# Optimization experiments

Measured on AMD Instinct MI355X. Metric: run time of the kernel, lower is better.

Reference implementation:

```python
import jax, jax.numpy as jnp
import numpy as np

H = 128  # hidden size
D = 257  # input size


def _lstm(x, h0, c0, Wih, Whh, bih, bhh):
    """Single-layer batch-first LSTM, PyTorch gate order (i, f, g, o).
    x: [N, T, D_in]; h0, c0: [N, H]. Returns (ys [N,T,H], hT, cT)."""
    # Precompute the input contribution for all timesteps at once.
    pre = jnp.einsum('ntd,gd->ntg', x, Wih) + bih + bhh  # [N, T, 4H]

    def step(carry, g_t):
        h, c = carry
        gates = g_t + h @ Whh.T  # [N, 4H]
        i, f, g, o = jnp.split(gates, 4, axis=-1)
        c = jax.nn.sigmoid(f) * c + jax.nn.sigmoid(i) * jnp.tanh(g)
        h = jax.nn.sigmoid(o) * jnp.tanh(c)
        return (h, c), h

    (hT, cT), ys = jax.lax.scan(step, (h0, c0), jnp.swapaxes(pre, 0, 1))
    return jnp.swapaxes(ys, 0, 1), hT, cT


def setup_inputs() -> dict:
    key = jax.random.key(0)
    ks = jax.random.split(key, 12)
    N, T = 64, 1000
    s1 = 1.0 / np.sqrt(H)
    inp = {
        'x': jax.random.normal(ks[0], (N, T, D), jnp.float32),
        'in_states': jax.random.normal(ks[1], (1, 4 * N, H), jnp.float32),
        'Wih1': jax.random.uniform(ks[2], (4 * H, D), jnp.float32, -s1, s1),
        'Whh1': jax.random.uniform(ks[3], (4 * H, H), jnp.float32, -s1, s1),
        'bih1': jax.random.uniform(ks[4], (4 * H,), jnp.float32, -s1, s1),
        'bhh1': jax.random.uniform(ks[5], (4 * H,), jnp.float32, -s1, s1),
        'Wih2': jax.random.uniform(ks[6], (4 * H, H), jnp.float32, -s1, s1),
        'Whh2': jax.random.uniform(ks[7], (4 * H, H), jnp.float32, -s1, s1),
        'bih2': jax.random.uniform(ks[8], (4 * H,), jnp.float32, -s1, s1),
        'bhh2': jax.random.uniform(ks[9], (4 * H,), jnp.float32, -s1, s1),
        'Wd': jax.random.uniform(ks[10], (D, H), jnp.float32, -s1, s1),
        'bd': jax.random.uniform(ks[11], (D,), jnp.float32, -s1, s1),
    }
    return inp


def reference(x, in_states, Wih1, Whh1, bih1, bhh1, Wih2, Whh2, bih2, bhh2, Wd, bd):
    # in_states: [1, 4N, H] -> four [1, N, H] chunks: h1, c1, h2, c2
    h1_in, c1_in, h2_in, c2_in = jnp.split(in_states, 4, axis=1)
    x1, h1, c1 = _lstm(x, h1_in[0], c1_in[0], Wih1, Whh1, bih1, bhh1)
    # dropout is identity in eval/streaming inference
    x2, h2, c2 = _lstm(x1, h2_in[0], c2_in[0], Wih2, Whh2, bih2, bhh2)
    mask = jax.nn.sigmoid(jnp.einsum('nth,dh->ntd', x2, Wd) + bd)
    out_states = jnp.concatenate([h1[None], c1[None], h2[None], c2[None]], axis=1)
    return mask, out_states
```

## Files before the change

### kernel.cpp

```cpp
#include <hip/hip_runtime.h>
#include <hip/hip_bf16.h>
#include <math.h>

#define NBATCH 64
#define TSEQ   1000
#define DIN    257
#define HID    128
#define GATES  512
#define CH     8
#define NCHUNK 125

typedef _Float16 h2    __attribute__((ext_vector_type(2)));
typedef _Float16 h4    __attribute__((ext_vector_type(4)));
typedef _Float16 half8 __attribute__((ext_vector_type(8)));
typedef float    f32x4 __attribute__((ext_vector_type(4)));

__device__ __forceinline__ float fast_sigmoid(float x) {
    return __builtin_amdgcn_rcpf(1.f + __expf(-x));
}
__device__ __forceinline__ float fast_tanh(float x) {
    const float e = __expf(2.f * x);
    return 1.f - 2.f * __builtin_amdgcn_rcpf(e + 1.f);
}
__device__ __forceinline__ void wait_flag(const int* f, int need) {
    while (__hip_atomic_load(f, __ATOMIC_ACQUIRE, __HIP_MEMORY_SCOPE_AGENT) < need)
        __builtin_amdgcn_s_sleep(2);
}

#define BM 128
#define BN 64
#define BK 64
#define LDK 88

template<int ACT>
__global__ __launch_bounds__(256) void gemm_mfma(
    const float* __restrict__ A, const float* __restrict__ W,
    const float* __restrict__ b1, const float* __restrict__ b2,
    float* __restrict__ C, int M, int K, int Ncols)
{
    __shared__ _Float16 As[BM][LDK];
    __shared__ _Float16 Ws[BN][LDK];

    const int tid  = threadIdx.x;
    const int wave = tid >> 6;
    const int lane = tid & 63;
    const int r    = lane & 15;
    const int q    = lane >> 4;
    const int m0   = blockIdx.y * BM;
    const int n0   = blockIdx.x * BN;
    const int wm   = (wave >> 1) * 64;
    const int wn   = (wave & 1) * 32;

    const int r16 = tid >> 4;
    const int c4  = (tid & 15) * 4;

    f32x4 acc[4][2];
#pragma unroll
    for (int i = 0; i < 4; ++i)
#pragma unroll
        for (int j = 0; j < 2; ++j) acc[i][j] = f32x4{0.f, 0.f, 0.f, 0.f};

    for (int kc = 0; kc < K; kc += BK) {
        const int kg = kc + c4;
        const bool vec_ok = (kg + 4 <= K);

#pragma unroll
        for (int it = 0; it < 8; ++it) {
            const int row = it * 16 + r16;
            const float* src = A + (size_t)(m0 + row) * K + kg;
            _Float16 tmp[4];
            if (vec_ok) {
                const float4 u = *(const float4*)src;
                tmp[0] = (_Float16)u.x; tmp[1] = (_Float16)u.y;
                tmp[2] = (_Float16)u.z; tmp[3] = (_Float16)u.w;
            } else {
#pragma unroll
                for (int j = 0; j < 4; ++j)
                    tmp[j] = (kg + j < K) ? (_Float16)src[j] : (_Float16)0.f;
            }
            *(h4*)&As[row][c4] = *(h4*)tmp;
        }
#pragma unroll
        for (int it = 0; it < 4; ++it) {
            const int row  = it * 16 + r16;
            const int wrow = n0 + row;
            _Float16 tmp[4] = {(_Float16)0.f, (_Float16)0.f, (_Float16)0.f, (_Float16)0.f};
            if (wrow < Ncols) {
                const float* src = W + (size_t)wrow * K + kg;
                if (vec_ok) {
                    const float4 u = *(const float4*)src;
                    tmp[0] = (_Float16)u.x; tmp[1] = (_Float16)u.y;
                    tmp[2] = (_Float16)u.z; tmp[3] = (_Float16)u.w;
                } else {
#pragma unroll
                    for (int j = 0; j < 4; ++j)
                        tmp[j] = (kg + j < K) ? (_Float16)src[j] : (_Float16)0.f;
                }
            }
            *(h4*)&Ws[row][c4] = *(h4*)tmp;
        }
        __syncthreads();

#pragma unroll
        for (int s = 0; s < 2; ++s) {
            const int kb = s * 32 + q * 8;
            half8 af[4], wfr[2];
#pragma unroll
            for (int i = 0; i < 4; ++i)
                af[i] = *(const half8*)&As[wm + i * 16 + r][kb];
#pragma unroll
            for (int j = 0; j < 2; ++j)
                wfr[j] = *(const half8*)&Ws[wn + j * 16 + r][kb];
#pragma unroll
            for (int i = 0; i < 4; ++i)
#pragma unroll
                for (int j = 0; j < 2; ++j)
                    acc[i][j] = __builtin_amdgcn_mfma_f32_16x16x32_f16(
                        af[i], wfr[j], acc[i][j], 0, 0, 0);
        }
        __syncthreads();
    }

#pragma unroll
    for (int i = 0; i < 4; ++i) {
#pragma unroll
        for (int j = 0; j < 2; ++j) {
            const int col = n0 + wn + j * 16 + r;
            if (col < Ncols) {
                const float bias = b1[col] + (b2 ? b2[col] : 0.f);
#pragma unroll
                for (int reg = 0; reg < 4; ++reg) {
                    const int row = m0 + wm + i * 16 + q * 4 + reg;
                    float v = acc[i][j][reg] + bias;
                    if (ACT == 1) v = fast_sigmoid(v);
                    C[(size_t)row * Ncols + col] = v;
                }
            }
        }
    }
}

__global__ __launch_bounds__(256, 1) void lstm_mega(
    float* preA,
    const float* __restrict__ states_in,
    const float* __restrict__ Whh1, const float* __restrict__ Whh2,
    const float* __restrict__ Wih2, const float* __restrict__ bih2,
    const float* __restrict__ bhh2,
    float* __restrict__ h2seq,
    float* __restrict__ states_out, int* __restrict__ flags)
{
    const int layer = blockIdx.x >> 6;
    const int n     = blockIdx.x & 63;
    const int tid   = threadIdx.x;
    const int w     = tid >> 6;
    const int lane  = tid & 63;
    const int r     = lane & 15;
    const int q     = lane >> 4;
    const int b     = q & 1;
    const int j     = 32 * w + 16 * b + r;
    const int h_row0 = layer ? 128 : 0;

    __shared__ __align__(16) _Float16 hbuf[2][HID];
    __shared__ __align__(16) _Float16 h1ck[2][CH][136];

    const float* Whh = layer ? Whh2 : Whh1;
    half8 wf[4][2][4];
#pragma unroll
    for (int g = 0; g < 4; ++g) {
#pragma unroll
        for (int b2 = 0; b2 < 2; ++b2) {
            const float* src = Whh + (size_t)(128 * g + 32 * w + 16 * b2 + r) * HID + q * 8;
#pragma unroll
            for (int s = 0; s < 4; ++s) {
                const float4 u0 = *(const float4*)(src + s * 32);
                const float4 u1 = *(const float4*)(src + s * 32 + 4);
                half8 tf;
                tf[0] = (_Float16)u0.x; tf[1] = (_Float16)u0.y;
                tf[2] = (_Float16)u0.z; tf[3] = (_Float16)u0.w;
                tf[4] = (_Float16)u1.x; tf[5] = (_Float16)u1.y;
                tf[6] = (_Float16)u1.z; tf[7] = (_Float16)u1.w;
                wf[g][b2][s] = tf;
            }
        }
    }

    half8 wih[8][4];
    float bias2v[8];
    if (layer == 0) {
#pragma unroll
        for (int fi = 0; fi < 8; ++fi) {
            const int row = 128 * w + 16 * fi + r;
            const float* src = Wih2 + (size_t)row * HID + q * 8;
#pragma unroll
            for (int s = 0; s < 4; ++s) {
                const float4 u0 = *(const float4*)(src + s * 32);
                const float4 u1 = *(const float4*)(src + s * 32 + 4);
                half8 tf;
                tf[0] = (_Float16)u0.x; tf[1] = (_Float16)u0.y;
                tf[2] = (_Float16)u0.z; tf[3] = (_Float16)u0.w;
                tf[4] = (_Float16)u1.x; tf[5] = (_Float16)u1.y;
                tf[6] = (_Float16)u1.z; tf[7] = (_Float16)u1.w;
                wih[fi][s] = tf;
            }
            bias2v[fi] = bih2[row] + bhh2[row];
        }
    }

    float c_r = states_in[(size_t)(h_row0 + 64 + n) * HID + j];
    if (tid < HID)
        hbuf[0][tid] = (_Float16)states_in[(size_t)(h_row0 + n) * HID + tid];
    __syncthreads();

    if (layer) wait_flag(flags + n, 2);

    const float* pre_n = preA + (size_t)n * TSEQ * GATES;
    float pc0 = pre_n[j],           pc1 = pre_n[j + 128];
    float pc2 = pre_n[j + 256],     pc3 = pre_n[j + 384];
    float pn0 = pre_n[GATES + j],       pn1 = pre_n[GATES + j + 128];
    float pn2 = pre_n[GATES + j + 256], pn3 = pre_n[GATES + j + 384];

    int cur = 0;
    for (int t = 0; t < TSEQ; ++t) {
        if (layer && t && !(t & 7)) {
            int need = (t >> 3) + 2;
            if (need > NCHUNK) need = NCHUNK;
            wait_flag(flags + n, need);
        }

        const float p0 = pc0, p1 = pc1, p2 = pc2, p3 = pc3;
        pc0 = pn0; pc1 = pn1; pc2 = pn2; pc3 = pn3;
        if (t + 2 < TSEQ) {
            const float* pp = pre_n + (size_t)(t + 2) * GATES + j;
            pn0 = pp[0]; pn1 = pp[128]; pn2 = pp[256]; pn3 = pp[384];
        }

        half8 hx[4];
#pragma unroll
        for (int s = 0; s < 4; ++s)
            hx[s] = *(const half8*)&hbuf[cur][s * 32 + q * 8];

        f32x4 acc[4][2];
        const f32x4 Z = {0.f, 0.f, 0.f, 0.f};
#pragma unroll
        for (int g = 0; g < 4; ++g)
#pragma unroll
            for (int b2 = 0; b2 < 2; ++b2)
                acc[g][b2] = __builtin_amdgcn_mfma_f32_16x16x32_f16(
                    hx[0], wf[g][b2][0], Z, 0, 0, 0);
#pragma unroll
        for (int s = 1; s < 4; ++s)
#pragma unroll
            for (int g = 0; g < 4; ++g)
#pragma unroll
                for (int b2 = 0; b2 < 2; ++b2)
                    acc[g][b2] = __builtin_amdgcn_mfma_f32_16x16x32_f16(
                        hx[s], wf[g][b2][s], acc[g][b2], 0, 0, 0);

        const float A0 = (b ? acc[0][1][0] : acc[0][0][0]) + p0;
        const float A1 = (b ? acc[1][1][0] : acc[1][0][0]) + p1;
        const float A2 = (b ? acc[2][1][0] : acc[2][0][0]) + p2;
        const float A3 = (b ? acc[3][1][0] : acc[3][0][0]) + p3;

        const float gi = fast_sigmoid(A0);
        const float gf = fast_sigmoid(A1);
        const float gg = fast_tanh(A2);
        const float go = fast_sigmoid(A3);

        const float cn = gf * c_r + gi * gg;
        const float hh = go * fast_tanh(cn);
        c_r = cn;

        if (q < 2) {
            hbuf[cur ^ 1][j] = (_Float16)hh;
            if (t == TSEQ - 1)
                states_out[(size_t)(h_row0 + 64 + n) * HID + j] = cn;
        } else {
            if (layer == 0)
                h1ck[(t >> 3) & 1][t & 7][j] = (_Float16)hh;
            else
                h2seq[((size_t)n * TSEQ + t) * HID + j] = hh;
            if (t == TSEQ - 1)
                states_out[(size_t)(h_row0 + n) * HID + j] = hh;
        }
        __syncthreads();

        if (layer == 0 && (t & 7) == 7) {
            const int c = t >> 3;
            if (c > 0 && tid == 0) {
                __threadfence();
                __hip_atomic_store(flags + n, c, __ATOMIC_RELAXED, __HIP_MEMORY_SCOPE_AGENT);
            }
            const int cb = c & 1;
            half8 ax[4];
#pragma unroll
            for (int s = 0; s < 4; ++s)
                ax[s] = *(const half8*)&h1ck[cb][r & 7][s * 32 + q * 8];
            f32x4 gacc[8];
            const f32x4 GZ = {0.f, 0.f, 0.f, 0.f};
#pragma unroll
            for (int fi = 0; fi < 8; ++fi)
                gacc[fi] = __builtin_amdgcn_mfma_f32_16x16x32_f16(
                    ax[0], wih[fi][0], GZ, 0, 0, 0);
#pragma unroll
            for (int s = 1; s < 4; ++s)
#pragma unroll
                for (int fi = 0; fi < 8; ++fi)
                    gacc[fi] = __builtin_amdgcn_mfma_f32_16x16x32_f16(
                        ax[s], wih[fi][s], gacc[fi], 0, 0, 0);
            if (q < 2) {
                float* dst0 = preA + ((size_t)n * TSEQ + (t - 7 + 4 * q)) * GATES + 128 * w + r;
#pragma unroll
                for (int fi = 0; fi < 8; ++fi)
#pragma unroll
                    for (int reg = 0; reg < 4; ++reg)
                        dst0[(size_t)reg * GATES + 16 * fi] = gacc[fi][reg] + bias2v[fi];
            }
        }
        cur ^= 1;
    }

    if (layer == 0) {
        __syncthreads();
        if (tid == 0) {
            __threadfence();
            __hip_atomic_store(flags + n, NCHUNK, __ATOMIC_RELAXED, __HIP_MEMORY_SCOPE_AGENT);
        }
    }
}

extern "C" void kernel_launch(void* const* d_in, const int* in_sizes, int n_in,
                              void* d_out, int out_size, void* d_ws, size_t ws_size,
                              hipStream_t stream)
{
    const float* x     = (const float*)d_in[0];
    const float* st_in = (const float*)d_in[1];
    const float* Wih1  = (const float*)d_in[2];
    const float* Whh1  = (const float*)d_in[3];
    const float* bih1  = (const float*)d_in[4];
    const float* bhh1  = (const float*)d_in[5];
    const float* Wih2  = (const float*)d_in[6];
    const float* Whh2  = (const float*)d_in[7];
    const float* bih2  = (const float*)d_in[8];
    const float* bhh2  = (const float*)d_in[9];
    const float* Wd    = (const float*)d_in[10];
    const float* bd    = (const float*)d_in[11];

    float* out_mask   = (float*)d_out;
    float* out_states = (float*)d_out + (size_t)NBATCH * TSEQ * DIN;

    const int M = NBATCH * TSEQ;
    float* bufA = (float*)d_ws;
    float* bufB = bufA + (size_t)M * GATES;

    int* flags = (int*)((float*)d_out + (size_t)NBATCH * TSEQ * DIN) - 64;
    hipMemsetAsync(flags, 0, 64 * sizeof(int), stream);

    gemm_mfma<0><<<dim3(GATES / BN, M / BM), 256, 0, stream>>>(
        x, Wih1, bih1, bhh1, bufA, M, DIN, GATES);

    lstm_mega<<<128, 256, 0, stream>>>(
        bufA, st_in, Whh1, Whh2, Wih2, bih2, bhh2, bufB, out_states, flags);

    gemm_mfma<1><<<dim3((DIN + BN - 1) / BN, M / BM), 256, 0, stream>>>(
        bufB, Wd, bd, nullptr, out_mask, M, HID, DIN);
}
```

Baseline: 1.267 ms.

## Move layer-2 input projection into layer-2 blocks with 40-step chunks

```diff
diff --git a/kernel.cpp b/kernel.cpp
--- a/kernel.cpp
+++ b/kernel.cpp
@@ -7,8 +7,8 @@
 #define DIN    257
 #define HID    128
 #define GATES  512
-#define CH     8
-#define NCHUNK 125
+#define CH     40
+#define NCHUNK 25
 
 typedef _Float16 h2    __attribute__((ext_vector_type(2)));
 typedef _Float16 h4    __attribute__((ext_vector_type(4)));
@@ -25,6 +25,16 @@
 __device__ __forceinline__ void wait_flag(const int* f, int need) {
     while (__hip_atomic_load(f, __ATOMIC_ACQUIRE, __HIP_MEMORY_SCOPE_AGENT) < need)
         __builtin_amdgcn_s_sleep(2);
+}
+__device__ __forceinline__ half8 cvt8(const float* p) {
+    const float4 a = *(const float4*)p;
+    const float4 b = *(const float4*)(p + 4);
+    half8 t;
+    t[0] = (_Float16)a.x; t[1] = (_Float16)a.y;
+    t[2] = (_Float16)a.z; t[3] = (_Float16)a.w;
+    t[4] = (_Float16)b.x; t[5] = (_Float16)b.y;
+    t[6] = (_Float16)b.z; t[7] = (_Float16)b.w;
+    return t;
 }
 
 #define BM 128
@@ -141,11 +151,11 @@
 }
 
 __global__ __launch_bounds__(256, 1) void lstm_mega(
-    float* preA,
-    const float* __restrict__ states_in,
+    const float* __restrict__ pre1, const float* __restrict__ states_in,
     const float* __restrict__ Whh1, const float* __restrict__ Whh2,
     const float* __restrict__ Wih2, const float* __restrict__ bih2,
     const float* __restrict__ bhh2,
+    _Float16* __restrict__ h1g,
     float* __restrict__ h2seq,
     float* __restrict__ states_out, int* __restrict__ flags)
 {
@@ -161,47 +171,28 @@
     const int h_row0 = layer ? 128 : 0;
 
     __shared__ __align__(16) _Float16 hbuf[2][HID];
-    __shared__ __align__(16) _Float16 h1ck[2][CH][136];
+    __shared__ __align__(16) float pre2ck[CH][GATES + 4];
 
     const float* Whh = layer ? Whh2 : Whh1;
     half8 wf[4][2][4];
 #pragma unroll
-    for (int g = 0; g < 4; ++g) {
+    for (int g = 0; g < 4; ++g)
 #pragma unroll
         for (int b2 = 0; b2 < 2; ++b2) {
             const float* src = Whh + (size_t)(128 * g + 32 * w + 16 * b2 + r) * HID + q * 8;
 #pragma unroll
-            for (int s = 0; s < 4; ++s) {
-                const float4 u0 = *(const float4*)(src + s * 32);
-                const float4 u1 = *(const float4*)(src + s * 32 + 4);
-                half8 tf;
-                tf[0] = (_Float16)u0.x; tf[1] = (_Float16)u0.y;
-                tf[2] = (_Float16)u0.z; tf[3] = (_Float16)u0.w;
-                tf[4] = (_Float16)u1.x; tf[5] = (_Float16)u1.y;
-                tf[6] = (_Float16)u1.z; tf[7] = (_Float16)u1.w;
-                wf[g][b2][s] = tf;
-            }
-        }
-    }
+            for (int s = 0; s < 4; ++s) wf[g][b2][s] = cvt8(src + s * 32);
+        }
 
     half8 wih[8][4];
     float bias2v[8];
-    if (layer == 0) {
+    if (layer == 1) {
 #pragma unroll
         for (int fi = 0; fi < 8; ++fi) {
             const int row = 128 * w + 16 * fi + r;
             const float* src = Wih2 + (size_t)row * HID + q * 8;
 #pragma unroll
-            for (int s = 0; s < 4; ++s) {
-                const float4 u0 = *(const float4*)(src + s * 32);
-                const float4 u1 = *(const float4*)(src + s * 32 + 4);
-                half8 tf;
-                tf[0] = (_Float16)u0.x; tf[1] = (_Float16)u0.y;
-                tf[2] = (_Float16)u0.z; tf[3] = (_Float16)u0.w;
-                tf[4] = (_Float16)u1.x; tf[5] = (_Float16)u1.y;
-                tf[6] = (_Float16)u1.z; tf[7] = (_Float16)u1.w;
-                wih[fi][s] = tf;
-            }
+            for (int s = 0; s < 4; ++s) wih[fi][s] = cvt8(src + s * 32);
             bias2v[fi] = bih2[row] + bhh2[row];
         }
     }
@@ -211,27 +202,67 @@
         hbuf[0][tid] = (_Float16)states_in[(size_t)(h_row0 + n) * HID + tid];
     __syncthreads();
 
-    if (layer) wait_flag(flags + n, 2);
-
-    const float* pre_n = preA + (size_t)n * TSEQ * GATES;
-    float pc0 = pre_n[j],           pc1 = pre_n[j + 128];
-    float pc2 = pre_n[j + 256],     pc3 = pre_n[j + 384];
-    float pn0 = pre_n[GATES + j],       pn1 = pre_n[GATES + j + 128];
-    float pn2 = pre_n[GATES + j + 256], pn3 = pre_n[GATES + j + 384];
-
-    int cur = 0;
+    const float* pre_n = pre1 + (size_t)n * TSEQ * GATES;
+    float pc0 = 0.f, pc1 = 0.f, pc2 = 0.f, pc3 = 0.f;
+    float pn0 = 0.f, pn1 = 0.f, pn2 = 0.f, pn3 = 0.f;
+    if (layer == 0) {
+        pc0 = pre_n[j];           pc1 = pre_n[j + 128];
+        pc2 = pre_n[j + 256];     pc3 = pre_n[j + 384];
+        pn0 = pre_n[GATES + j];       pn1 = pre_n[GATES + j + 128];
+        pn2 = pre_n[GATES + j + 256]; pn3 = pre_n[GATES + j + 384];
+    }
+
+    const f32x4 Z = {0.f, 0.f, 0.f, 0.f};
+    int cur = 0, ts = 0, ck = 0;
+
     for (int t = 0; t < TSEQ; ++t) {
-        if (layer && t && !(t & 7)) {
-            int need = (t >> 3) + 2;
-            if (need > NCHUNK) need = NCHUNK;
-            wait_flag(flags + n, need);
-        }
-
-        const float p0 = pc0, p1 = pc1, p2 = pc2, p3 = pc3;
-        pc0 = pn0; pc1 = pn1; pc2 = pn2; pc3 = pn3;
-        if (t + 2 < TSEQ) {
-            const float* pp = pre_n + (size_t)(t + 2) * GATES + j;
-            pn0 = pp[0]; pn1 = pp[128]; pn2 = pp[256]; pn3 = pp[384];
+        if (layer == 1 && ts == 0) {
+            wait_flag(flags + n, ck + 1);
+            const _Float16* hbase = h1g + ((size_t)n * TSEQ + (size_t)ck * CH) * HID;
+#pragma unroll
+            for (int mt = 0; mt < 3; ++mt) {
+                const int mrow = (mt < 2) ? (mt * 16 + r) : (32 + (r & 7));
+                const _Float16* src = hbase + (size_t)mrow * HID + q * 8;
+                half8 ax[4];
+#pragma unroll
+                for (int s = 0; s < 4; ++s)
+                    ax[s] = *(const half8*)(src + s * 32);
+                f32x4 gacc[8];
+#pragma unroll
+                for (int fi = 0; fi < 8; ++fi)
+                    gacc[fi] = __builtin_amdgcn_mfma_f32_16x16x32_f16(
+                        ax[0], wih[fi][0], Z, 0, 0, 0);
+#pragma unroll
+                for (int s = 1; s < 4; ++s)
+#pragma unroll
+                    for (int fi = 0; fi < 8; ++fi)
+                        gacc[fi] = __builtin_amdgcn_mfma_f32_16x16x32_f16(
+                            ax[s], wih[fi][s], gacc[fi], 0, 0, 0);
+                if (mt < 2 || q < 2) {
+#pragma unroll
+                    for (int fi = 0; fi < 8; ++fi)
+#pragma unroll
+                        for (int reg = 0; reg < 4; ++reg)
+                            pre2ck[mt * 16 + 4 * q + reg][128 * w + 16 * fi + r] =
+                                gacc[fi][reg] + bias2v[fi];
+                }
+            }
+            __syncthreads();
+        }
+
+        float p0, p1, p2, p3;
+        if (layer == 0) {
+            p0 = pc0; p1 = pc1; p2 = pc2; p3 = pc3;
+            pc0 = pn0; pc1 = pn1; pc2 = pn2; pc3 = pn3;
+            if (t + 2 < TSEQ) {
+                const float* pp = pre_n + (size_t)(t + 2) * GATES + j;
+                pn0 = pp[0]; pn1 = pp[128]; pn2 = pp[256]; pn3 = pp[384];
+            }
+        } else {
+            p0 = pre2ck[ts][j];
+            p1 = pre2ck[ts][j + 128];
+            p2 = pre2ck[ts][j + 256];
+            p3 = pre2ck[ts][j + 384];
         }
 
         half8 hx[4];
@@ -240,7 +271,6 @@
             hx[s] = *(const half8*)&hbuf[cur][s * 32 + q * 8];
 
         f32x4 acc[4][2];
-        const f32x4 Z = {0.f, 0.f, 0.f, 0.f};
 #pragma unroll
         for (int g = 0; g < 4; ++g)
 #pragma unroll
@@ -276,7 +306,7 @@
                 states_out[(size_t)(h_row0 + 64 + n) * HID + j] = cn;
         } else {
             if (layer == 0)
-                h1ck[(t >> 3) & 1][t & 7][j] = (_Float16)hh;
+                h1g[((size_t)n * TSEQ + t) * HID + j] = (_Float16)hh;
             else
                 h2seq[((size_t)n * TSEQ + t) * HID + j] = hh;
             if (t == TSEQ - 1)
@@ -284,47 +314,14 @@
         }
         __syncthreads();
 
-        if (layer == 0 && (t & 7) == 7) {
-            const int c = t >> 3;
-            if (c > 0 && tid == 0) {
-                __threadfence();
-                __hip_atomic_store(flags + n, c, __ATOMIC_RELAXED, __HIP_MEMORY_SCOPE_AGENT);
-            }
-            const int cb = c & 1;
-            half8 ax[4];
-#pragma unroll
-            for (int s = 0; s < 4; ++s)
-                ax[s] = *(const half8*)&h1ck[cb][r & 7][s * 32 + q * 8];
-            f32x4 gacc[8];
-            const f32x4 GZ = {0.f, 0.f, 0.f, 0.f};
-#pragma unroll
-            for (int fi = 0; fi < 8; ++fi)
-                gacc[fi] = __builtin_amdgcn_mfma_f32_16x16x32_f16(
-                    ax[0], wih[fi][0], GZ, 0, 0, 0);
-#pragma unroll
-            for (int s = 1; s < 4; ++s)
-#pragma unroll
-                for (int fi = 0; fi < 8; ++fi)
-                    gacc[fi] = __builtin_amdgcn_mfma_f32_16x16x32_f16(
-                        ax[s], wih[fi][s], gacc[fi], 0, 0, 0);
-            if (q < 2) {
-                float* dst0 = preA + ((size_t)n * TSEQ + (t - 7 + 4 * q)) * GATES + 128 * w + r;
-#pragma unroll
-                for (int fi = 0; fi < 8; ++fi)
-#pragma unroll
-                    for (int reg = 0; reg < 4; ++reg)
-                        dst0[(size_t)reg * GATES + 16 * fi] = gacc[fi][reg] + bias2v[fi];
-            }
-        }
+        if (layer == 0 && ts == CH - 1 && tid == 0) {
+            __threadfence();
+            __hip_atomic_store(flags + n, ck + 1,
+                               __ATOMIC_RELAXED, __HIP_MEMORY_SCOPE_AGENT);
+        }
+
+        if (++ts == CH) { ts = 0; ++ck; }
         cur ^= 1;
-    }
-
-    if (layer == 0) {
-        __syncthreads();
-        if (tid == 0) {
-            __threadfence();
-            __hip_atomic_store(flags + n, NCHUNK, __ATOMIC_RELAXED, __HIP_MEMORY_SCOPE_AGENT);
-        }
     }
 }
 
@@ -352,14 +349,15 @@
     float* bufA = (float*)d_ws;
     float* bufB = bufA + (size_t)M * GATES;
 
-    int* flags = (int*)((float*)d_out + (size_t)NBATCH * TSEQ * DIN) - 64;
+    _Float16* h1g = (_Float16*)out_mask;
+    int* flags = (int*)(out_mask + (size_t)NBATCH * TSEQ * DIN) - 64;
     hipMemsetAsync(flags, 0, 64 * sizeof(int), stream);
 
     gemm_mfma<0><<<dim3(GATES / BN, M / BM), 256, 0, stream>>>(
         x, Wih1, bih1, bhh1, bufA, M, DIN, GATES);
 
     lstm_mega<<<128, 256, 0, stream>>>(
-        bufA, st_in, Whh1, Whh2, Wih2, bih2, bhh2, bufB, out_states, flags);
+        bufA, st_in, Whh1, Whh2, Wih2, bih2, bhh2, h1g, bufB, out_states, flags);
 
     gemm_mfma<1><<<dim3((DIN + BN - 1) / BN, M / BM), 256, 0, stream>>>(
         bufB, Wd, bd, nullptr, out_mask, M, HID, DIN);
```

Result: faster. 1.097 ms (-13.4%).
